# Kernel optimization log

Hardware: AMD Instinct MI355X
Metric: run time of the kernel (lower is better)

The kernel has to match this reference:

```python
import jax, jax.numpy as jnp
import numpy as np

EPS = 1e-8
UNTANH = 0.5                       # hp UNTANH (blend factor, assumed)
BUNTANH_SCALE = (2.0 + 2.0 ** 0.5) ** 0.5  # sqrt(2 + sqrt(2)) from source
C_MOMENT = 0.99                    # hp c_moment
A_VARIANCE = 0.02                  # hp a_variance
SINKHORN_ITERS = 8


def rms_norm(x, axes):
    ms = jnp.mean(x * x, axis=axes, keepdims=True)
    return x * jax.lax.rsqrt(ms + EPS)


def buntanh(x):
    # blended un-tanh: untanh * identity + (1-untanh) * tanh, rescaled
    return BUNTANH_SCALE * (UNTANH * x + (1.0 - UNTANH) * jnp.tanh(x))


def sinkhorn_knopp(A, n_iter=SINKHORN_ITERS):
    A = jnp.maximum(A, 0.0) + EPS
    def body(A, _):
        A = A / jnp.sum(A, axis=-1, keepdims=True)  # row normalize
        A = A / jnp.sum(A, axis=-2, keepdims=True)  # col normalize
        return A, None
    A, _ = jax.lax.scan(body, A, None, length=n_iter)
    return A


def setup_inputs() -> dict:
    key = jax.random.key(0)
    ks = jax.random.split(key, 8)
    B, N, D, IN_DIM = 4, 1024, 128, 8192
    inv_sqrt_d = 1.0 / np.sqrt(D)
    return {
        "state": jax.random.normal(ks[0], (B, N, D), jnp.float32) * 0.1,
        "output": jax.random.normal(ks[1], (B, N, D), jnp.float32) * 0.1,
        "w1": jax.random.normal(ks[2], (B, N, D, D), jnp.float32) * inv_sqrt_d,
        "w2": jax.random.normal(ks[3], (B, N, D, D), jnp.float32) * inv_sqrt_d,
        "w3": jax.random.normal(ks[4], (B, N, D, D), jnp.float32) * inv_sqrt_d,
        "A_ema": jax.random.normal(ks[5], (B, N, N), jnp.float32) * 0.01,
        "env_input": jax.random.normal(ks[6], (B, IN_DIM), jnp.float32),
        "noise": jax.random.normal(ks[7], (B, N, D), jnp.float32),
    }


def reference(state, output, w1, w2, w3, A_ema, env_input, noise):
    B, N, D = state.shape
    input_dim = env_input.shape[1]
    num_in = -(-input_dim // D)  # ceil

    # first-call mask/EMA adjustment (num_input_nodes change branch)
    A_mask = jnp.ones((N, N), dtype=state.dtype).at[:num_in, :].set(0.0)
    A_ema = A_ema.at[:, num_in, :num_in].add(3.0 / num_in)

    # per-node batched small GEMMs + custom activation
    Q = buntanh(jnp.einsum('bnd,bndk->bnk', state, w3))
    K = buntanh(jnp.einsum('bnd,bndk->bnk', state, w2))
    prediction = buntanh(jnp.einsum('bnd,bndk->bnk', state, w1))

    # QK^T adjacency, rms-normed over full [N,N]
    raw_A = jnp.einsum('bnk,bmk->bnm', Q, K) / jnp.sqrt(jnp.asarray(D, state.dtype))
    raw_A = rms_norm(raw_A, (-2, -1))

    # EMA (non-first step) + input-node masking
    new_A_ema = (A_ema * C_MOMENT + raw_A * (1.0 - C_MOMENT)) * A_mask

    # doubly-stochastic projection, thresholded sparsification, re-project
    dsA = sinkhorn_knopp(new_A_ema)
    baseline = 1.0 / (N + 1.0)
    sparse_A = jnp.where(dsA > baseline, dsA, 0.0)
    A = sinkhorn_knopp(sparse_A) * A_mask

    # boredom noise scaled by variance deficit (torch var is unbiased)
    var = jnp.var(A, axis=(-2, -1), keepdims=True, ddof=1)
    vd = jax.nn.relu(A_VARIANCE - var)
    V = output + vd * noise

    # message passing + softsign, overwrite input-node rows with env input
    target = jax.nn.soft_sign(jnp.einsum('bnm,bmd->bnd', A, V))
    pad = num_in * D - input_dim
    env = jnp.pad(env_input, ((0, 0), (0, pad))).reshape(B, num_in, D)
    target = target.at[:, :num_in, :].set(env)

    out = jnp.concatenate([target, prediction], axis=-1)  # [B,N,2D]
    return out, A
```

## Files before the change

### kernel.cpp

```cpp
#include <hip/hip_runtime.h>
#include <math.h>

#define NB 4
#define NN 1024
#define ND 128
#define NUM_IN 64
#define F_EPS 1e-8f
#define BT_SCALE 1.8477590650225735f
#define INV_SQRT_D 0.08838834764831844f
#define BASELINE (1.0f/1025.0f)
#define OUT_STRIDE 256
#define A_OFF 1048576

__device__ __forceinline__ float buntanh_f(float x) {
    return BT_SCALE * (0.5f * x + 0.5f * tanhf(x));
}
__device__ __forceinline__ float wave_sum(float v) {
    #pragma unroll
    for (int off = 32; off > 0; off >>= 1) v += __shfl_xor(v, off, 64);
    return v;
}
__device__ __forceinline__ float bflo(unsigned u) { return __uint_as_float(u << 16); }
__device__ __forceinline__ float bfhi(unsigned u) { return __uint_as_float(u & 0xffff0000u); }
__device__ __forceinline__ unsigned bf_rne(float f) {
    unsigned x = __float_as_uint(f);
    return (x + 0x7fffu + ((x >> 16) & 1u)) >> 16;
}
__device__ __forceinline__ unsigned bf_pack(float lo, float hi) {
    return bf_rne(lo) | (bf_rne(hi) << 16);
}

typedef float f32x4 __attribute__((ext_vector_type(4)));
__device__ __forceinline__ float4 ntload4(const float4* p) {
    f32x4 v = __builtin_nontemporal_load((const f32x4*)p);
    return make_float4(v.x, v.y, v.z, v.w);
}

__device__ __forceinline__ void pred_node(
    const int node, const float* __restrict__ state,
    const float* __restrict__ w1, float* __restrict__ dout)
{
    __shared__ float4 pred_red[8][32];
    const int t = threadIdx.x;
    const int g = t >> 5, m = t & 31;
    const float4* w4 = (const float4*)(w1 + ((size_t)node << 14));
    const float* srow = state + ((size_t)node << 7);
    float4 acc = make_float4(0.f, 0.f, 0.f, 0.f);
    #pragma unroll
    for (int h = 0; h < 2; ++h) {
        float4 wv[8];
        #pragma unroll
        for (int i = 0; i < 8; ++i) wv[i] = ntload4(&w4[(h*8 + i)*256 + t]);
        #pragma unroll
        for (int i = 0; i < 8; ++i) {
            const float s = srow[(h*8 + i)*8 + g];
            acc.x += s*wv[i].x; acc.y += s*wv[i].y;
            acc.z += s*wv[i].z; acc.w += s*wv[i].w;
        }
    }
    pred_red[g][m] = acc;
    __syncthreads();
    if (t < 32) {
        float4 o = pred_red[0][t];
        #pragma unroll
        for (int gg = 1; gg < 8; ++gg) {
            const float4 r = pred_red[gg][t];
            o.x += r.x; o.y += r.y; o.z += r.z; o.w += r.w;
        }
        o.x = buntanh_f(o.x); o.y = buntanh_f(o.y);
        o.z = buntanh_f(o.z); o.w = buntanh_f(o.w);
        *(float4*)(dout + (size_t)node * OUT_STRIDE + ND + 4*t) = o;
    }
}

__global__ __launch_bounds__(256, 8) void qk_kernel(
    const float* __restrict__ state,
    const float* __restrict__ w2,
    const float* __restrict__ w3,
    float* __restrict__ Qg,
    float* __restrict__ Kg)
{
    const int blk = blockIdx.x;
    const int node = ((blk & 7) << 9) | (blk >> 3);

    __shared__ float s_state[ND];
    __shared__ float4 red[2][8][32];

    const int t = threadIdx.x;
    if (t < 32) ((float4*)s_state)[t] =
        ((const float4*)(state + ((size_t)node << 7)))[t];
    __syncthreads();

    const int g = t >> 5, m = t & 31;

    auto do_mat = [&](const float* wbase, int q) {
        const float4* w4 = (const float4*)(wbase + ((size_t)node << 14));
        float4 wv[8];
        float4 acc = make_float4(0.f, 0.f, 0.f, 0.f);
        #pragma unroll
        for (int i = 0; i < 8; ++i) wv[i] = ntload4(&w4[i*256 + t]);
        #pragma unroll
        for (int i = 0; i < 8; ++i) {
            const float s = s_state[i*8 + g];
            acc.x += s*wv[i].x; acc.y += s*wv[i].y;
            acc.z += s*wv[i].z; acc.w += s*wv[i].w;
        }
        #pragma unroll
        for (int i = 0; i < 8; ++i) wv[i] = ntload4(&w4[(8+i)*256 + t]);
        #pragma unroll
        for (int i = 0; i < 8; ++i) {
            const float s = s_state[(8+i)*8 + g];
            acc.x += s*wv[i].x; acc.y += s*wv[i].y;
            acc.z += s*wv[i].z; acc.w += s*wv[i].w;
        }
        red[q][g][m] = acc;
    };
    do_mat(w2, 0);
    do_mat(w3, 1);
    __syncthreads();

    if (t < 64) {
        const int q = t >> 5, mm = t & 31;
        float4 o = red[q][0][mm];
        #pragma unroll
        for (int gg = 1; gg < 8; ++gg) {
            const float4 r = red[q][gg][mm];
            o.x += r.x; o.y += r.y; o.z += r.z; o.w += r.w;
        }
        o.x = buntanh_f(o.x); o.y = buntanh_f(o.y);
        o.z = buntanh_f(o.z); o.w = buntanh_f(o.w);
        float* base = (q == 0) ? Kg : Qg;
        *(float4*)(base + ((size_t)node << 7) + 4*mm) = o;
    }
}

__global__ __launch_bounds__(256) void qk2_kernel(
    const float* __restrict__ Qg, const float* __restrict__ Kg,
    unsigned* __restrict__ rawbf, float* __restrict__ reds,
    const float* __restrict__ state, const float* __restrict__ w1,
    float* __restrict__ dout, int predBase)
{
    if (blockIdx.x >= 4096) {
        pred_node(predBase + (int)blockIdx.x - 4096, state, w1, dout);
        return;
    }
    const int b = blockIdx.x >> 10;
    const int tile = blockIdx.x & 1023;
    const int tr = tile >> 5, tc = tile & 31;

    __shared__ float Qs[32][132];
    __shared__ float Ks[32][136];
    __shared__ float wr4[4];

    const int t = threadIdx.x;
    for (int i = t; i < 1024; i += 256) {
        const int r = i >> 5, q = i & 31;
        *(float4*)&Qs[r][q*4] = *(const float4*)(Qg + (((size_t)(b*NN + tr*32 + r)) << 7) + q*4);
        *(float4*)&Ks[r][q*4] = *(const float4*)(Kg + (((size_t)(b*NN + tc*32 + r)) << 7) + q*4);
    }
    __syncthreads();

    const int ty = t >> 4;
    const int tx = t & 15;
    float a00=0.f, a01=0.f, a10=0.f, a11=0.f;
    #pragma unroll
    for (int dq = 0; dq < 32; ++dq) {
        const float4 q0 = *(const float4*)&Qs[ty][dq*4];
        const float4 q1 = *(const float4*)&Qs[ty+16][dq*4];
        const float4 k0 = *(const float4*)&Ks[2*tx][dq*4];
        const float4 k1 = *(const float4*)&Ks[2*tx+1][dq*4];
        a00 += q0.x*k0.x + q0.y*k0.y + q0.z*k0.z + q0.w*k0.w;
        a01 += q0.x*k1.x + q0.y*k1.y + q0.z*k1.z + q0.w*k1.w;
        a10 += q1.x*k0.x + q1.y*k0.y + q1.z*k0.z + q1.w*k0.w;
        a11 += q1.x*k1.x + q1.y*k1.y + q1.z*k1.z + q1.w*k1.w;
    }
    a00 *= INV_SQRT_D; a01 *= INV_SQRT_D; a10 *= INV_SQRT_D; a11 *= INV_SQRT_D;

    unsigned* r0p = rawbf + (((size_t)(b*NN + tr*32 + ty)) << 9) + tc*16;
    unsigned* r1p = rawbf + (((size_t)(b*NN + tr*32 + ty + 16)) << 9) + tc*16;
    r0p[tx] = bf_pack(a00, a01);
    r1p[tx] = bf_pack(a10, a11);

    float ssq = a00*a00 + a01*a01 + a10*a10 + a11*a11;
    ssq = wave_sum(ssq);
    if ((t & 63) == 0) wr4[t >> 6] = ssq;
    __syncthreads();
    if (t == 0) atomicAdd(&reds[b], wr4[0]+wr4[1]+wr4[2]+wr4[3]);
}

__global__ __launch_bounds__(256) void emaT_kernel(
    const unsigned* __restrict__ rawbf, const float* __restrict__ A_ema,
    const float* __restrict__ reds,
    unsigned* __restrict__ M0, unsigned* __restrict__ M0T,
    float* __restrict__ SR,
    const float* __restrict__ state, const float* __restrict__ w1,
    float* __restrict__ dout, int predBase)
{
    if (blockIdx.x >= 1024) {
        pred_node(predBase + (int)blockIdx.x - 1024, state, w1, dout);
        return;
    }
    const int b = blockIdx.x >> 8;
    const int tile = blockIdx.x & 255;
    const int tr = tile >> 4, tc = tile & 15;
    const int R0 = tr << 6, C0 = tc << 6;

    __shared__ float st[64][65];
    __shared__ float s_part[64][5];

    const int t = threadIdx.x;
    const int r = t >> 2, q = t & 3;
    const int row = R0 + r;
    const float scale = rsqrtf(reds[b] * (1.0f/1048576.0f) + F_EPS);

    const unsigned* rawrow = rawbf + (((size_t)(b*NN + row)) << 9) + tc*8*4;
    const uint4 u0 = ((const uint4*)rawrow)[q*2];
    const uint4 u1 = ((const uint4*)rawrow)[q*2 + 1];
    float rv[16];
    rv[0]=bflo(u0.x); rv[1]=bfhi(u0.x); rv[2]=bflo(u0.y); rv[3]=bfhi(u0.y);
    rv[4]=bflo(u0.z); rv[5]=bfhi(u0.z); rv[6]=bflo(u0.w); rv[7]=bfhi(u0.w);
    rv[8]=bflo(u1.x); rv[9]=bfhi(u1.x); rv[10]=bflo(u1.y); rv[11]=bfhi(u1.y);
    rv[12]=bflo(u1.z); rv[13]=bfhi(u1.z); rv[14]=bflo(u1.w); rv[15]=bfhi(u1.w);

    const float* emarow = A_ema + (((size_t)(b*NN + row)) << 10) + C0 + q*16;
    float s = 0.f;
    #pragma unroll
    for (int j = 0; j < 4; ++j) {
        const float4 e = ((const float4*)emarow)[j];
        float ev[4] = {e.x, e.y, e.z, e.w};
        #pragma unroll
        for (int k = 0; k < 4; ++k) {
            const int e_idx = j*4 + k;
            const int c = C0 + q*16 + e_idx;
            float em = ev[k];
            if (row == NUM_IN && c < NUM_IN) em += 3.0f / NUM_IN;
            float v = em * 0.99f + rv[e_idx] * scale * 0.01f;
            if (row < NUM_IN) v = 0.f;
            v = fmaxf(v, 0.f) + F_EPS;
            rv[e_idx] = v;
            st[r][q*16 + e_idx] = v;
            s += v;
        }
    }
    s_part[r][q] = s;

    unsigned* m0row = M0 + (((size_t)(b*NN + row)) << 9) + tc*8*4;
    uint4 o0, o1;
    o0.x = bf_pack(rv[0],rv[1]);  o0.y = bf_pack(rv[2],rv[3]);
    o0.z = bf_pack(rv[4],rv[5]);  o0.w = bf_pack(rv[6],rv[7]);
    o1.x = bf_pack(rv[8],rv[9]);  o1.y = bf_pack(rv[10],rv[11]);
    o1.z = bf_pack(rv[12],rv[13]); o1.w = bf_pack(rv[14],rv[15]);
    ((uint4*)m0row)[q*2]     = o0;
    ((uint4*)m0row)[q*2 + 1] = o1;
    __syncthreads();

    if (t < 64) {
        const float rs = s_part[t][0] + s_part[t][1] + s_part[t][2] + s_part[t][3];
        atomicAdd(&SR[b*NN + R0 + t], rs);
    }

    const int cT = t >> 2;
    float tv[16];
    #pragma unroll
    for (int k = 0; k < 16; ++k) tv[k] = st[q*16 + k][cT];
    uint4 w0, w1v;
    w0.x = bf_pack(tv[0],tv[1]);  w0.y = bf_pack(tv[2],tv[3]);
    w0.z = bf_pack(tv[4],tv[5]);  w0.w = bf_pack(tv[6],tv[7]);
    w1v.x = bf_pack(tv[8],tv[9]);  w1v.y = bf_pack(tv[10],tv[11]);
    w1v.z = bf_pack(tv[12],tv[13]); w1v.w = bf_pack(tv[14],tv[15]);
    unsigned* mtrow = M0T + (((size_t)(b*NN + C0 + cT)) << 9) + tr*8*4;
    ((uint4*)mtrow)[q*2]     = w0;
    ((uint4*)mtrow)[q*2 + 1] = w1v;
}

template<bool INV_IN>
__global__ __launch_bounds__(256) void mv_kernel(
    const unsigned* __restrict__ Abf, const float* __restrict__ x,
    float* __restrict__ y,
    const float* __restrict__ state, const float* __restrict__ w1,
    float* __restrict__ dout, int predBase)
{
    const int blk = blockIdx.x;
    if (blk >= 256) {
        pred_node(predBase + blk - 256, state, w1, dout);
        return;
    }
    const int lp  = ((blk & 7) << 5) | (blk >> 3);
    const int b   = lp >> 6;
    const int r0  = (lp & 63) << 4;
    const int t = threadIdx.x;
    const int w = t >> 6, l = t & 63;

    const float4* xb = (const float4*)(x + (b << 10));
    float4 x0 = xb[2*l], x1 = xb[2*l+1], x2 = xb[128+2*l], x3 = xb[129+2*l];
    if (INV_IN) {
        x0.x=1.f/x0.x; x0.y=1.f/x0.y; x0.z=1.f/x0.z; x0.w=1.f/x0.w;
        x1.x=1.f/x1.x; x1.y=1.f/x1.y; x1.z=1.f/x1.z; x1.w=1.f/x1.w;
        x2.x=1.f/x2.x; x2.y=1.f/x2.y; x2.z=1.f/x2.z; x2.w=1.f/x2.w;
        x3.x=1.f/x3.x; x3.y=1.f/x3.y; x3.z=1.f/x3.z; x3.w=1.f/x3.w;
    }

    #pragma unroll
    for (int r = 0; r < 4; ++r) {
        const int row = r0 + (w << 2) + r;
        const unsigned* rp = Abf + (((size_t)((b << 10) + row)) << 9);
        const uint4 v0 = ((const uint4*)rp)[l];
        const uint4 v1 = ((const uint4*)rp)[64 + l];
        float a = bflo(v0.x)*x0.x + bfhi(v0.x)*x0.y
                + bflo(v0.y)*x0.z + bfhi(v0.y)*x0.w
                + bflo(v0.z)*x1.x + bfhi(v0.z)*x1.y
                + bflo(v0.w)*x1.z + bfhi(v0.w)*x1.w
                + bflo(v1.x)*x2.x + bfhi(v1.x)*x2.y
                + bflo(v1.y)*x2.z + bfhi(v1.y)*x2.w
                + bflo(v1.z)*x3.x + bfhi(v1.z)*x3.y
                + bflo(v1.w)*x3.z + bfhi(v1.w)*x3.w;
        a = wave_sum(a);
        if (l == 0) y[(b << 10) + row] = 1.0f / a;
    }
}

__global__ __launch_bounds__(256) void thresh_kernel(
    const unsigned* __restrict__ M0, const unsigned* __restrict__ M0T,
    const float* __restrict__ r8, const float* __restrict__ c8,
    unsigned* __restrict__ A1, unsigned* __restrict__ A1T,
    float* __restrict__ SR2,
    const float* __restrict__ state, const float* __restrict__ w1,
    float* __restrict__ dout, int predBase)
{
    if (blockIdx.x >= 256) {
        pred_node(predBase + (int)blockIdx.x - 256, state, w1, dout);
        return;
    }
    const int t = threadIdx.x;
    const int b = blockIdx.x >> 6;
    const int g0 = (blockIdx.x & 63) << 4;
    const int w = t >> 6, l = t & 63;
    const bool doA1 = (w < 2);
    const int wr = doA1 ? w : (w - 2);
    const unsigned* src = doA1 ? M0 : M0T;
    unsigned*       dst = doA1 ? A1 : A1T;
    const float* rowS = doA1 ? r8 : c8;
    const float* colS = doA1 ? c8 : r8;

    const float4* cb = (const float4*)(colS + (b << 10));
    const float4 c0 = cb[2*l], c1 = cb[2*l+1], c2 = cb[128+2*l], c3 = cb[129+2*l];
    const float cm[16] = {c0.x,c0.y,c0.z,c0.w, c1.x,c1.y,c1.z,c1.w,
                          c2.x,c2.y,c2.z,c2.w, c3.x,c3.y,c3.z,c3.w};

    for (int rr = 0; rr < 8; ++rr) {
        const int row = g0 + wr*8 + rr;
        const float ri = rowS[(b << 10) + row];
        const unsigned* rp = src + (((size_t)(b*NN + row)) << 9);
        const uint4 v0 = ((const uint4*)rp)[l];
        const uint4 v1 = ((const uint4*)rp)[64 + l];
        float e[16];
        e[0]=bflo(v0.x); e[1]=bfhi(v0.x); e[2]=bflo(v0.y); e[3]=bfhi(v0.y);
        e[4]=bflo(v0.z); e[5]=bfhi(v0.z); e[6]=bflo(v0.w); e[7]=bfhi(v0.w);
        e[8]=bflo(v1.x); e[9]=bfhi(v1.x); e[10]=bflo(v1.y); e[11]=bfhi(v1.y);
        e[12]=bflo(v1.z); e[13]=bfhi(v1.z); e[14]=bflo(v1.w); e[15]=bfhi(v1.w);
        float s = 0.f;
        #pragma unroll
        for (int j = 0; j < 16; ++j) {
            const float d = e[j] * ri * cm[j];
            e[j] = (d > BASELINE ? d : 0.f) + F_EPS;
            s += e[j];
        }
        uint4 o0, o1;
        o0.x = bf_pack(e[0],e[1]);  o0.y = bf_pack(e[2],e[3]);
        o0.z = bf_pack(e[4],e[5]);  o0.w = bf_pack(e[6],e[7]);
        o1.x = bf_pack(e[8],e[9]);  o1.y = bf_pack(e[10],e[11]);
        o1.z = bf_pack(e[12],e[13]); o1.w = bf_pack(e[14],e[15]);
        unsigned* op = dst + (((size_t)(b*NN + row)) << 9);
        ((uint4*)op)[l] = o0;
        ((uint4*)op)[64 + l] = o1;
        if (doA1) {
            s = wave_sum(s);
            if (l == 0) SR2[b*NN + row] = s;
        }
    }
}

__global__ __launch_bounds__(256) void fin_kernel(
    const unsigned* __restrict__ A1, const float* __restrict__ r8,
    const float* __restrict__ c8, float* __restrict__ reds,
    float* __restrict__ dout,
    const float* __restrict__ state, const float* __restrict__ w1,
    int predBase)
{
    if (blockIdx.x >= 256) {
        pred_node(predBase + (int)blockIdx.x - 256, state, w1, dout);
        return;
    }
    __shared__ float wred[8];
    const int t = threadIdx.x;
    const int b = blockIdx.x >> 6;
    const int g0 = (blockIdx.x & 63) << 4;
    const int w = t >> 6, l = t & 63;

    const float4* cb = (const float4*)(c8 + (b << 10));
    const float4 c0 = cb[2*l], c1 = cb[2*l+1], c2 = cb[128+2*l], c3 = cb[129+2*l];
    const float cm[16] = {c0.x,c0.y,c0.z,c0.w, c1.x,c1.y,c1.z,c1.w,
                          c2.x,c2.y,c2.z,c2.w, c3.x,c3.y,c3.z,c3.w};

    float s1 = 0.f, s2 = 0.f;
    for (int rr = 0; rr < 4; ++rr) {
        const int row = g0 + w*4 + rr;
        float* Arow = dout + A_OFF + (((size_t)(b*NN + row)) << 10);
        if (row < NUM_IN) {
            const float4 z = make_float4(0.f,0.f,0.f,0.f);
            ((float4*)Arow)[2*l] = z;       ((float4*)Arow)[2*l+1] = z;
            ((float4*)Arow)[128+2*l] = z;   ((float4*)Arow)[129+2*l] = z;
        } else {
            const float ri = r8[(b << 10) + row];
            const unsigned* rp = A1 + (((size_t)(b*NN + row)) << 9);
            const uint4 v0 = ((const uint4*)rp)[l];
            const uint4 v1 = ((const uint4*)rp)[64 + l];
            float e[16];
            e[0]=bflo(v0.x); e[1]=bfhi(v0.x); e[2]=bflo(v0.y); e[3]=bfhi(v0.y);
            e[4]=bflo(v0.z); e[5]=bfhi(v0.z); e[6]=bflo(v0.w); e[7]=bfhi(v0.w);
            e[8]=bflo(v1.x); e[9]=bfhi(v1.x); e[10]=bflo(v1.y); e[11]=bfhi(v1.y);
            e[12]=bflo(v1.z); e[13]=bfhi(v1.z); e[14]=bflo(v1.w); e[15]=bfhi(v1.w);
            #pragma unroll
            for (int j = 0; j < 16; ++j) {
                e[j] = e[j] * ri * cm[j];
                s1 += e[j]; s2 += e[j]*e[j];
            }
            ((float4*)Arow)[2*l]     = make_float4(e[0],e[1],e[2],e[3]);
            ((float4*)Arow)[2*l+1]   = make_float4(e[4],e[5],e[6],e[7]);
            ((float4*)Arow)[128+2*l] = make_float4(e[8],e[9],e[10],e[11]);
            ((float4*)Arow)[129+2*l] = make_float4(e[12],e[13],e[14],e[15]);
        }
    }
    s1 = wave_sum(s1); s2 = wave_sum(s2);
    if (l == 0) { wred[w] = s1; wred[4 + w] = s2; }
    __syncthreads();
    if (t == 0) {
        atomicAdd(&reds[4 + b], wred[0]+wred[1]+wred[2]+wred[3]);
        atomicAdd(&reds[8 + b], wred[4]+wred[5]+wred[6]+wred[7]);
    }
}

__global__ __launch_bounds__(256) void vbuild_kernel(
    const float* __restrict__ outp, const float* __restrict__ noise,
    const float* __restrict__ reds, float* __restrict__ V)
{
    const int i = blockIdx.x * 256 + threadIdx.x;
    const int b = i >> 15;
    const float Mn = 1048576.f;
    const float S1 = reds[4 + b], S2 = reds[8 + b];
    const float var = (S2 - S1*S1/Mn) / (Mn - 1.f);
    const float vd = fmaxf(0.02f - var, 0.f);
    const float4 o = ((const float4*)outp)[i];
    const float4 n = ((const float4*)noise)[i];
    ((float4*)V)[i] = make_float4(o.x + vd*n.x, o.y + vd*n.y,
                                  o.z + vd*n.z, o.w + vd*n.w);
}

__global__ __launch_bounds__(256) void av_part(
    const float* __restrict__ A, const float* __restrict__ V,
    float* __restrict__ P,
    const float* __restrict__ state, const float* __restrict__ w1,
    float* __restrict__ dout, int predBase)
{
    if (blockIdx.x >= 960) {
        pred_node(predBase + (int)blockIdx.x - 960, state, w1, dout);
        return;
    }
    const int bid = blockIdx.x;
    const int ks = bid & 3;
    const int rt = (bid >> 2) % 60;
    const int b  = bid / 240;
    const int r0 = NUM_IN + rt * 16;
    const int mc0 = ks << 8;
    const int t = threadIdx.x;
    const int d = t & 127, rg = t >> 7;
    const int rowb = r0 + rg*8;

    float acc[8] = {0.f,0.f,0.f,0.f,0.f,0.f,0.f,0.f};
    const float* Vb = V + ((size_t)b << 17) + ((size_t)mc0 << 7) + d;
    const float* Ab = A + (((size_t)(b*NN + rowb)) << 10) + mc0;

    #pragma unroll 4
    for (int mq = 0; mq < 64; ++mq) {
        const float v0 = Vb[(mq*4 + 0) << 7];
        const float v1 = Vb[(mq*4 + 1) << 7];
        const float v2 = Vb[(mq*4 + 2) << 7];
        const float v3 = Vb[(mq*4 + 3) << 7];
        #pragma unroll
        for (int k = 0; k < 8; ++k) {
            const float4 a = *(const float4*)(Ab + ((size_t)k << 10) + mq*4);
            acc[k] += a.x*v0 + a.y*v1 + a.z*v2 + a.w*v3;
        }
    }
    #pragma unroll
    for (int k = 0; k < 8; ++k) {
        const int ridx = rt*16 + rg*8 + k;
        P[(((size_t)(ks*NB + b)) * 960 + ridx) * 128 + d] = acc[k];
    }
}

__global__ __launch_bounds__(256) void av_fin(
    const float* __restrict__ P, const float* __restrict__ env,
    float* __restrict__ dout)
{
    const int t = threadIdx.x;
    int bid = blockIdx.x;
    if (bid < 128) {
        const int idx = bid*256 + t;
        const int b = idx >> 13, off = idx & 8191;
        const int r = off >> 7, d = off & 127;
        dout[((size_t)(b*NN + r)) * OUT_STRIDE + d] = env[idx];
        return;
    }
    bid -= 128;
    const int idx = bid*256 + t;
    const int d = idx & 127;
    const int rd = idx >> 7;
    const int b = rd / 960;
    const int ridx = rd - b*960;
    const float s = P[idx] + P[idx + 491520] + P[idx + 2*491520] + P[idx + 3*491520];
    dout[((size_t)(b*NN + NUM_IN + ridx)) * OUT_STRIDE + d] = s / (1.f + fabsf(s));
}

extern "C" void kernel_launch(void* const* d_in, const int* in_sizes, int n_in,
                              void* d_out, int out_size, void* d_ws, size_t ws_size,
                              hipStream_t stream)
{
    (void)in_sizes; (void)n_in; (void)out_size; (void)ws_size;
    const float* state = (const float*)d_in[0];
    const float* outp  = (const float*)d_in[1];
    const float* w1    = (const float*)d_in[2];
    const float* w2    = (const float*)d_in[3];
    const float* w3    = (const float*)d_in[4];
    const float* A_ema = (const float*)d_in[5];
    const float* env   = (const float*)d_in[6];
    const float* noise = (const float*)d_in[7];
    float* dout = (float*)d_out;

    unsigned* M0  = (unsigned*)(dout + A_OFF);
    unsigned* M0T = M0 + 2097152;

    float*    Qg   = (float*)d_ws;
    float*    Kg   = Qg + 524288;
    float*    Vg   = Kg + 524288;
    unsigned* raw  = (unsigned*)(Vg + 524288);
    unsigned* A1   = raw;
    unsigned* A1T  = raw + 2097152;
    float*    Pp   = (float*)A1T;
    float*    SR1  = (float*)(A1T + 2097152);
    float*    reds = SR1 + 4096;
    float*    SC1  = reds + 16;
    float*    SR2  = SC1 + 4096;
    float*    SC2  = SR2 + 4096;
    float*    RV1  = SC2 + 4096;
    float*    RV2  = RV1 + 4096;

    hipMemsetAsync(SR1, 0, (4096 + 16) * sizeof(float), stream);

    qk_kernel<<<dim3(NB*NN), dim3(256), 0, stream>>>(state, w2, w3, Qg, Kg);

    int pb = 0;
    qk2_kernel<<<dim3(4096 + 512), dim3(256), 0, stream>>>(
        Qg, Kg, raw, reds, state, w1, dout, pb);
    pb += 512;

    emaT_kernel<<<dim3(1024 + 512), dim3(256), 0, stream>>>(
        raw, A_ema, reds, M0, M0T, SR1, state, w1, dout, pb);
    pb += 512;

    mv_kernel<true ><<<dim3(256 + 64), dim3(256), 0, stream>>>(
        M0T, SR1, SC1, state, w1, dout, pb);
    pb += 64;
    for (int k = 1; k < 15; ++k) {
        if (k & 1)
            mv_kernel<false><<<dim3(256 + 64), dim3(256), 0, stream>>>(
                M0, SC1, RV1, state, w1, dout, pb);
        else
            mv_kernel<false><<<dim3(256 + 64), dim3(256), 0, stream>>>(
                M0T, RV1, SC1, state, w1, dout, pb);
        pb += 64;
    }

    thresh_kernel<<<dim3(256 + 384), dim3(256), 0, stream>>>(
        M0, M0T, RV1, SC1, A1, A1T, SR2, state, w1, dout, pb);
    pb += 384;

    mv_kernel<true ><<<dim3(256 + 64), dim3(256), 0, stream>>>(
        A1T, SR2, SC2, state, w1, dout, pb);
    pb += 64;
    for (int k = 1; k < 15; ++k) {
        if (k & 1)
            mv_kernel<false><<<dim3(256 + 64), dim3(256), 0, stream>>>(
                A1, SC2, RV2, state, w1, dout, pb);
        else
            mv_kernel<false><<<dim3(256 + 64), dim3(256), 0, stream>>>(
                A1T, RV2, SC2, state, w1, dout, pb);
        pb += 64;
    }

    fin_kernel<<<dim3(256 + 384), dim3(256), 0, stream>>>(
        A1, RV2, SC2, reds, dout, state, w1, pb);
    pb += 384;

    vbuild_kernel<<<dim3(512), dim3(256), 0, stream>>>(outp, noise, reds, Vg);

    av_part<<<dim3(960 + 384), dim3(256), 0, stream>>>(
        dout + A_OFF, Vg, Pp, state, w1, dout, pb);
    pb += 384;

    av_fin<<<dim3(2048), dim3(256), 0, stream>>>(Pp, env, dout);
}
```

Measured before the change: 437.4 us.

## Fuse Sinkhorn matvec launches into a cooperative grid-synced kernel

Replaces the 30 separate per-iteration Sinkhorn matvec launches with two cooperative kernels that loop over all 15 half-iterations inside one launch. Iterations are separated by atomic-counter grid barriers, and the input vector is staged in swizzled shared memory. The prediction-node work that used to ride along in the matvec launches is moved into the other kernels' extra blocks. This removes per-launch overhead and tail effects, at the cost of spin-wait barriers and a dependence on all 256 blocks being co-resident.

```diff
diff --git a/kernel.cpp b/kernel.cpp
--- a/kernel.cpp
+++ b/kernel.cpp
@@ -11,6 +11,8 @@
 #define BASELINE (1.0f/1025.0f)
 #define OUT_STRIDE 256
 #define A_OFF 1048576
+
+#define SWZ(c) ((((c) & 7) << 7) | ((c) >> 3))
 
 __device__ __forceinline__ float buntanh_f(float x) {
     return BT_SCALE * (0.5f * x + 0.5f * tanhf(x));
@@ -273,49 +275,62 @@
     ((uint4*)mtrow)[q*2 + 1] = w1v;
 }
 
-template<bool INV_IN>
-__global__ __launch_bounds__(256) void mv_kernel(
-    const unsigned* __restrict__ Abf, const float* __restrict__ x,
-    float* __restrict__ y,
-    const float* __restrict__ state, const float* __restrict__ w1,
-    float* __restrict__ dout, int predBase)
-{
+__global__ __launch_bounds__(1024) void sink_coop(
+    const unsigned* __restrict__ Mrow,
+    const unsigned* __restrict__ Mcol,
+    const float* __restrict__ s0,
+    float* __restrict__ cbuf, float* __restrict__ rbuf,
+    unsigned* __restrict__ cnt)
+{
+    __shared__ float xs[NN];
     const int blk = blockIdx.x;
-    if (blk >= 256) {
-        pred_node(predBase + blk - 256, state, w1, dout);
-        return;
-    }
-    const int lp  = ((blk & 7) << 5) | (blk >> 3);
-    const int b   = lp >> 6;
-    const int r0  = (lp & 63) << 4;
+    const int b = blk >> 6;
+    const int rbase = (blk & 63) << 4;
     const int t = threadIdx.x;
     const int w = t >> 6, l = t & 63;
-
-    const float4* xb = (const float4*)(x + (b << 10));
-    float4 x0 = xb[2*l], x1 = xb[2*l+1], x2 = xb[128+2*l], x3 = xb[129+2*l];
-    if (INV_IN) {
-        x0.x=1.f/x0.x; x0.y=1.f/x0.y; x0.z=1.f/x0.z; x0.w=1.f/x0.w;
-        x1.x=1.f/x1.x; x1.y=1.f/x1.y; x1.z=1.f/x1.z; x1.w=1.f/x1.w;
-        x2.x=1.f/x2.x; x2.y=1.f/x2.y; x2.z=1.f/x2.z; x2.w=1.f/x2.w;
-        x3.x=1.f/x3.x; x3.y=1.f/x3.y; x3.z=1.f/x3.z; x3.w=1.f/x3.w;
-    }
-
-    #pragma unroll
-    for (int r = 0; r < 4; ++r) {
-        const int row = r0 + (w << 2) + r;
-        const unsigned* rp = Abf + (((size_t)((b << 10) + row)) << 9);
+    const int row = rbase + w;
+
+    for (int p = 0; p < 15; ++p) {
+        const bool even = ((p & 1) == 0);
+        const unsigned* A = even ? Mcol : Mrow;
+        const float* xin = (p == 0) ? s0 : (even ? rbuf : cbuf);
+        float* yout = even ? cbuf : rbuf;
+
+        float xv = __hip_atomic_load(&xin[(b << 10) + t], __ATOMIC_RELAXED,
+                                     __HIP_MEMORY_SCOPE_AGENT);
+        if (p == 0) xv = 1.0f / xv;
+        xs[SWZ(t)] = xv;
+        __syncthreads();
+
+        const unsigned* rp = A + (((size_t)((b << 10) + row)) << 9);
         const uint4 v0 = ((const uint4*)rp)[l];
         const uint4 v1 = ((const uint4*)rp)[64 + l];
-        float a = bflo(v0.x)*x0.x + bfhi(v0.x)*x0.y
-                + bflo(v0.y)*x0.z + bfhi(v0.y)*x0.w
-                + bflo(v0.z)*x1.x + bfhi(v0.z)*x1.y
-                + bflo(v0.w)*x1.z + bfhi(v0.w)*x1.w
-                + bflo(v1.x)*x2.x + bfhi(v1.x)*x2.y
-                + bflo(v1.y)*x2.z + bfhi(v1.y)*x2.w
-                + bflo(v1.z)*x3.x + bfhi(v1.z)*x3.y
-                + bflo(v1.w)*x3.z + bfhi(v1.w)*x3.w;
+        const float* xA = &xs[l];
+        const float* xB = &xs[64 + l];
+        float a = bflo(v0.x)*xA[0<<7] + bfhi(v0.x)*xA[1<<7]
+                + bflo(v0.y)*xA[2<<7] + bfhi(v0.y)*xA[3<<7]
+                + bflo(v0.z)*xA[4<<7] + bfhi(v0.z)*xA[5<<7]
+                + bflo(v0.w)*xA[6<<7] + bfhi(v0.w)*xA[7<<7]
+                + bflo(v1.x)*xB[0<<7] + bfhi(v1.x)*xB[1<<7]
+                + bflo(v1.y)*xB[2<<7] + bfhi(v1.y)*xB[3<<7]
+                + bflo(v1.z)*xB[4<<7] + bfhi(v1.z)*xB[5<<7]
+                + bflo(v1.w)*xB[6<<7] + bfhi(v1.w)*xB[7<<7];
         a = wave_sum(a);
-        if (l == 0) y[(b << 10) + row] = 1.0f / a;
+        if (l == 0)
+            __hip_atomic_store(&yout[(b << 10) + row], 1.0f / a,
+                               __ATOMIC_RELAXED, __HIP_MEMORY_SCOPE_AGENT);
+        __syncthreads();
+
+        if (p < 14) {
+            if (t == 0) {
+                __hip_atomic_fetch_add(&cnt[p], 1u, __ATOMIC_ACQ_REL,
+                                       __HIP_MEMORY_SCOPE_AGENT);
+                while (__hip_atomic_load(&cnt[p], __ATOMIC_ACQUIRE,
+                                         __HIP_MEMORY_SCOPE_AGENT) < 256u)
+                    __builtin_amdgcn_s_sleep(2);
+            }
+            __syncthreads();
+        }
     }
 }
 
@@ -549,64 +564,54 @@
     float*    Pp   = (float*)A1T;
     float*    SR1  = (float*)(A1T + 2097152);
     float*    reds = SR1 + 4096;
-    float*    SC1  = reds + 16;
+    unsigned* cnt  = (unsigned*)(reds + 16);
+    float*    SC1  = (float*)(cnt + 32);
     float*    SR2  = SC1 + 4096;
     float*    SC2  = SR2 + 4096;
     float*    RV1  = SC2 + 4096;
     float*    RV2  = RV1 + 4096;
 
-    hipMemsetAsync(SR1, 0, (4096 + 16) * sizeof(float), stream);
+    hipMemsetAsync(SR1, 0, (4096 + 16 + 32) * sizeof(float), stream);
 
     qk_kernel<<<dim3(NB*NN), dim3(256), 0, stream>>>(state, w2, w3, Qg, Kg);
 
     int pb = 0;
-    qk2_kernel<<<dim3(4096 + 512), dim3(256), 0, stream>>>(
+    qk2_kernel<<<dim3(4096 + 1536), dim3(256), 0, stream>>>(
         Qg, Kg, raw, reds, state, w1, dout, pb);
+    pb += 1536;
+
+    emaT_kernel<<<dim3(1024 + 768), dim3(256), 0, stream>>>(
+        raw, A_ema, reds, M0, M0T, SR1, state, w1, dout, pb);
+    pb += 768;
+
+    {
+        void* args[] = { (void*)&M0, (void*)&M0T, (void*)&SR1,
+                         (void*)&SC1, (void*)&RV1, (void*)&cnt };
+        hipLaunchCooperativeKernel((void*)sink_coop, dim3(256), dim3(1024),
+                                   args, 0, stream);
+    }
+
+    thresh_kernel<<<dim3(256 + 768), dim3(256), 0, stream>>>(
+        M0, M0T, RV1, SC1, A1, A1T, SR2, state, w1, dout, pb);
+    pb += 768;
+
+    {
+        unsigned* cnt2 = cnt + 16;
+        void* args[] = { (void*)&A1, (void*)&A1T, (void*)&SR2,
+                         (void*)&SC2, (void*)&RV2, (void*)&cnt2 };
+        hipLaunchCooperativeKernel((void*)sink_coop, dim3(256), dim3(1024),
+                                   args, 0, stream);
+    }
+
+    fin_kernel<<<dim3(256 + 512), dim3(256), 0, stream>>>(
+        A1, RV2, SC2, reds, dout, state, w1, pb);
     pb += 512;
 
-    emaT_kernel<<<dim3(1024 + 512), dim3(256), 0, stream>>>(
-        raw, A_ema, reds, M0, M0T, SR1, state, w1, dout, pb);
+    vbuild_kernel<<<dim3(512), dim3(256), 0, stream>>>(outp, noise, reds, Vg);
+
+    av_part<<<dim3(960 + 512), dim3(256), 0, stream>>>(
+        dout + A_OFF, Vg, Pp, state, w1, dout, pb);
     pb += 512;
 
-    mv_kernel<true ><<<dim3(256 + 64), dim3(256), 0, stream>>>(
-        M0T, SR1, SC1, state, w1, dout, pb);
-    pb += 64;
-    for (int k = 1; k < 15; ++k) {
-        if (k & 1)
-            mv_kernel<false><<<dim3(256 + 64), dim3(256), 0, stream>>>(
-                M0, SC1, RV1, state, w1, dout, pb);
-        else
-            mv_kernel<false><<<dim3(256 + 64), dim3(256), 0, stream>>>(
-                M0T, RV1, SC1, state, w1, dout, pb);
-        pb += 64;
-    }
-
-    thresh_kernel<<<dim3(256 + 384), dim3(256), 0, stream>>>(
-        M0, M0T, RV1, SC1, A1, A1T, SR2, state, w1, dout, pb);
-    pb += 384;
-
-    mv_kernel<true ><<<dim3(256 + 64), dim3(256), 0, stream>>>(
-        A1T, SR2, SC2, state, w1, dout, pb);
-    pb += 64;
-    for (int k = 1; k < 15; ++k) {
-        if (k & 1)
-            mv_kernel<false><<<dim3(256 + 64), dim3(256), 0, stream>>>(
-                A1, SC2, RV2, state, w1, dout, pb);
-        else
-            mv_kernel<false><<<dim3(256 + 64), dim3(256), 0, stream>>>(
-                A1T, RV2, SC2, state, w1, dout, pb);
-        pb += 64;
-    }
-
-    fin_kernel<<<dim3(256 + 384), dim3(256), 0, stream>>>(
-        A1, RV2, SC2, reds, dout, state, w1, pb);
-    pb += 384;
-
-    vbuild_kernel<<<dim3(512), dim3(256), 0, stream>>>(outp, noise, reds, Vg);
-
-    av_part<<<dim3(960 + 384), dim3(256), 0, stream>>>(
-        dout + A_OFF, Vg, Pp, state, w1, dout, pb);
-    pb += 384;
-
     av_fin<<<dim3(2048), dim3(256), 0, stream>>>(Pp, env, dout);
 }
```

After: 624.2 us. 1.43x slower.
